# Performance work log

Measured on AMD Instinct MI355X. Metric: run time of the kernel, lower is better.

The kernel has to match this reference:

```python
import jax, jax.numpy as jnp
import numpy as np

D_MODEL = 512; D_STATE = 64; D_CONV = 4; EXPAND = 1; HEADDIM = 128; NGROUPS = 2; CHUNK = 256
D_INNER = EXPAND * (D_MODEL // 2)          # 256
NHEADS = D_INNER // HEADDIM                 # 2
CONV_DIM = D_INNER + 2 * NGROUPS * D_STATE  # 512
D_IN_PROJ = CONV_DIM + NHEADS               # 514

def silu(x):
    return x * jax.nn.sigmoid(x)

def conv1x1(x, w, b):
    # x: (b,c,h,w), w: (o,c)
    return jnp.einsum('bchw,oc->bohw', x, w) + b[None, :, None, None]

def dwconv3x3(x, w, b):
    # depthwise 3x3, SAME padding; w: (c,1,3,3)
    c = x.shape[1]
    y = jax.lax.conv_general_dilated(x, w, (1, 1), 'SAME', feature_group_count=c,
                                     dimension_numbers=('NCHW', 'OIHW', 'NCHW'))
    return y + b[None, :, None, None]

def causal_dwconv1d(x, w, b):
    # x: (b,L,c); w: (c,k). Torch pads k-1 both sides then slices [:L] -> causal left pad.
    k = w.shape[1]
    xp = jnp.pad(x, ((0, 0), (k - 1, 0), (0, 0))).transpose(0, 2, 1)  # (b,c,L+k-1)
    y = jax.lax.conv_general_dilated(xp, w[:, None, :], (1,), 'VALID',
                                     feature_group_count=w.shape[0],
                                     dimension_numbers=('NCH', 'OIH', 'NCH'))
    return y.transpose(0, 2, 1) + b

def axis_attn(x, qw, qb, fw, fb, axis):
    # DualAxisAggAttn single-axis step
    qkv = conv1x1(x, qw, qb)
    c = x.shape[1]
    q, k, v = qkv[:, :1], qkv[:, 1:1 + c], qkv[:, 1 + c:]
    dim = -1 if axis == 'W' else -2
    scores = jax.nn.softmax(q, axis=dim)
    ctx = jnp.sum(k * scores, axis=dim, keepdims=True)
    out = x + jax.nn.sigmoid(v) * ctx
    return conv1x1(out, fw, fb)

def segsum(x):
    # x: (...,T) -> (...,T,T) lower-triangular segment sums, -inf above diagonal
    T = x.shape[-1]
    cs = jnp.cumsum(x, -1)
    d = cs[..., :, None] - cs[..., None, :]
    mask = jnp.tril(jnp.ones((T, T), bool))
    return jnp.where(mask, d, -jnp.inf)

def ssd(X, A, B, C, chunk):
    # Mamba2 SSD chunked scan. X: (b,l,h,p) = x*dt; A: (b,l,h) = dt*A_head; B,C: (b,l,h,n)
    b, l, h, p = X.shape; n = B.shape[-1]; c = l // chunk
    X = X.reshape(b, c, chunk, h, p)
    B = B.reshape(b, c, chunk, h, n)
    C = C.reshape(b, c, chunk, h, n)
    A = A.reshape(b, c, chunk, h).transpose(0, 3, 1, 2)  # (b,h,c,L)
    Acs = jnp.cumsum(A, -1)
    L = jnp.exp(segsum(A))  # (b,h,c,L,L) intra-chunk decay
    Yd = jnp.einsum('bclhn,bcshn,bhcls,bcshp->bclhp', C, B, L, X)
    dec = jnp.exp(Acs[..., -1:] - Acs)
    st = jnp.einsum('bclhn,bhcl,bclhp->bchpn', B, dec, X)  # chunk end-states
    st = jnp.concatenate([jnp.zeros_like(st[:, :1]), st], 1)
    dchunk = jnp.exp(segsum(jnp.pad(Acs[..., -1], ((0, 0), (0, 0), (1, 0)))))
    st = jnp.einsum('bhzc,bchpn->bzhpn', dchunk, st)[:, :-1]  # states entering each chunk
    Yo = jnp.einsum('bclhn,bchpn,bhcl->bclhp', C, st, jnp.exp(Acs))
    return (Yd + Yo).reshape(b, l, h, p)

def setup_inputs() -> dict:
    key = jax.random.key(0)
    ks = jax.random.split(key, 12)
    s = 0.02
    p = {}
    p['u'] = jax.random.normal(ks[0], (8, D_MODEL, 64, 64), jnp.float32)
    p['sc_w1'] = jax.random.normal(ks[1], (D_MODEL, D_MODEL)) * s
    p['sc_b1'] = jnp.zeros((D_MODEL,))
    p['sc_wdw'] = jax.random.normal(ks[2], (D_MODEL, 1, 3, 3)) * s
    p['sc_bdw'] = jnp.zeros((D_MODEL,))
    p['sc_w2'] = jax.random.normal(ks[3], (D_INNER, D_MODEL)) * s
    p['sc_b2'] = jnp.zeros((D_INNER,))
    p['mc_w'] = jax.random.normal(ks[4], (D_INNER, D_MODEL)) * s
    p['mc_b'] = jnp.zeros((D_INNER,))
    p['qkvW_w'] = jax.random.normal(ks[5], (1 + 2 * D_INNER, D_INNER)) * s
    p['qkvW_b'] = jnp.zeros((1 + 2 * D_INNER,))
    p['qkvH_w'] = jax.random.normal(ks[6], (1 + 2 * D_INNER, D_INNER)) * s
    p['qkvH_b'] = jnp.zeros((1 + 2 * D_INNER,))
    p['fuseW_w'] = jax.random.normal(ks[7], (D_INNER, D_INNER)) * s
    p['fuseW_b'] = jnp.zeros((D_INNER,))
    p['fuseH_w'] = jax.random.normal(ks[8], (D_INNER, D_INNER)) * s
    p['fuseH_b'] = jnp.zeros((D_INNER,))
    p['in_proj_w'] = jax.random.normal(ks[9], (D_IN_PROJ, D_INNER)) * s
    p['conv1d_w'] = jax.random.normal(ks[10], (CONV_DIM, D_CONV)) * s
    p['conv1d_b'] = jnp.zeros((CONV_DIM,))
    dt = np.exp(np.linspace(np.log(1e-3), np.log(0.1), NHEADS))
    p['dt_bias'] = jnp.asarray(dt + np.log(-np.expm1(-dt)), jnp.float32)
    p['A_log'] = jnp.asarray(np.log(np.linspace(1.0, 16.0, NHEADS)), jnp.float32)
    p['D'] = jnp.ones((NHEADS,))
    p['norm_w'] = jnp.ones((D_INNER,))
    p['outp_w'] = jax.random.normal(ks[11], (D_MODEL, 2 * D_INNER)) * s
    p['outp_b'] = jnp.zeros((D_MODEL,))
    return p

def reference(u, sc_w1, sc_b1, sc_wdw, sc_bdw, sc_w2, sc_b2, mc_w, mc_b,
              qkvW_w, qkvW_b, qkvH_w, qkvH_b, fuseW_w, fuseW_b, fuseH_w, fuseH_b,
              in_proj_w, conv1d_w, conv1d_b, dt_bias, A_log, D, norm_w, outp_w, outp_b):
    b, _, H, W = u.shape
    # short_conv branch (light_ConvBlock: 1x1 -> dw3x3 -> 1x1, all SiLU; BN folded into bias)
    z = silu(conv1x1(u, sc_w1, sc_b1))
    z = silu(dwconv3x3(z, sc_wdw, sc_bdw))
    z = silu(conv1x1(z, sc_w2, sc_b2))
    # main branch
    x = silu(conv1x1(u, mc_w, mc_b))
    x = axis_attn(x, qkvW_w, qkvW_b, fuseW_w, fuseW_b, 'W')
    x = axis_attn(x, qkvH_w, qkvH_b, fuseH_w, fuseH_b, 'H')
    seqlen = H * W
    u2 = x.transpose(0, 2, 3, 1).reshape(b, seqlen, D_INNER)  # b (h w) c
    xbcdt = u2 @ in_proj_w.T  # (b,l,d_in_proj)
    xBC = xbcdt[..., :CONV_DIM]
    dt = jax.nn.softplus(xbcdt[..., CONV_DIM:] + dt_bias)  # (b,l,h)
    A = -jnp.exp(A_log)  # (h,)
    xBC = silu(causal_dwconv1d(xBC, conv1d_w, conv1d_b))
    xs = xBC[..., :D_INNER]
    Bs = xBC[..., D_INNER:D_INNER + NGROUPS * D_STATE].reshape(b, seqlen, NGROUPS, D_STATE)
    Cs = xBC[..., D_INNER + NGROUPS * D_STATE:].reshape(b, seqlen, NGROUPS, D_STATE)
    Xh = xs.reshape(b, seqlen, NHEADS, HEADDIM)
    rep = NHEADS // NGROUPS
    Bh = jnp.repeat(Bs, rep, axis=2)
    Ch = jnp.repeat(Cs, rep, axis=2)
    y = ssd(Xh * dt[..., None], dt * A[None, None, :], Bh, Ch, CHUNK)
    y = y + Xh * D[None, None, :, None]  # D skip connection
    y = y.reshape(b, seqlen, D_INNER)
    # RMSNormGated with z=None -> plain RMSNorm
    y = y * jax.lax.rsqrt(jnp.mean(y * y, -1, keepdims=True) + 1e-5) * norm_w
    y = y.reshape(b, H, W, D_INNER).transpose(0, 3, 1, 2)
    y = jnp.concatenate([z, y], axis=1)
    return conv1x1(y, outp_w, outp_b)
```

## Files before the change

kernel.cpp:

```cpp
#include <hip/hip_runtime.h>
#include <hip/hip_bf16.h>
#include <cstddef>
#include <cstdint>

#define PTOT 32768
#define HWSZ 4096

typedef __attribute__((ext_vector_type(8))) short bf16x8;
typedef __attribute__((ext_vector_type(4))) short s16x4;
typedef __attribute__((ext_vector_type(4))) float f32x4;

__device__ __forceinline__ float sigf(float x){ return 1.f/(1.f+__expf(-x)); }
__device__ __forceinline__ float siluf(float x){ return x*sigf(x); }
__device__ __forceinline__ short f2b(float x){
  __hip_bfloat16 h = __float2bfloat16(x);
  return *reinterpret_cast<short*>(&h);
}
__device__ __forceinline__ float b2f(short s){
  unsigned u = ((unsigned)(unsigned short)s) << 16;
  return __uint_as_float(u);
}

__device__ __forceinline__ void gload16(const void* g, void* l){
  __builtin_amdgcn_global_load_lds(
      (const __attribute__((address_space(1))) unsigned int*)g,
      (__attribute__((address_space(3))) unsigned int*)l, 16, 0, 0);
}

__global__ __launch_bounds__(256) void k_cvtw(
    const float* __restrict__ s0, const float* __restrict__ s1, const float* __restrict__ s2,
    const float* __restrict__ s3, const float* __restrict__ s4, const float* __restrict__ s5,
    const float* __restrict__ s6, const float* __restrict__ s7, const float* __restrict__ s8,
    short* __restrict__ dst){
  int idx = blockIdx.x*256 + threadIdx.x;
  const float* s; int off;
  if      (idx <  262144){ s=s0; off=idx; }
  else if (idx <  393216){ s=s1; off=idx- 262144; }
  else if (idx <  524288){ s=s2; off=idx- 393216; }
  else if (idx <  655616){ s=s3; off=idx- 524288; }
  else if (idx <  786944){ s=s4; off=idx- 655616; }
  else if (idx <  852480){ s=s5; off=idx- 786944; }
  else if (idx <  918016){ s=s6; off=idx- 852480; }
  else if (idx < 1049600){ s=s7; off=idx- 918016; }
  else if (idx < 1311744){ s=s8; off=idx-1049600; }
  else return;
  dst[idx] = f2b(s[off]);
}

__global__ __launch_bounds__(256) void k_transpose(const float* __restrict__ in, short* __restrict__ out){
  __shared__ float tile[64][33];
  int b = blockIdx.z;
  int c0 = blockIdx.y * 64;
  int s0 = blockIdx.x * 32;
  int tx = threadIdx.x, ty = threadIdx.y;
  const float* ip = in + ((size_t)b*512 + c0)*HWSZ + s0;
  for (int i = ty; i < 64; i += 8) tile[i][tx] = ip[(size_t)i*HWSZ + tx];
  __syncthreads();
  for (int i = ty; i < 32; i += 8){
    unsigned lo = (unsigned)(unsigned short)f2b(tile[2*tx][i]);
    unsigned hi = (unsigned)(unsigned short)f2b(tile[2*tx+1][i]);
    unsigned pk = lo | (hi<<16);
    *reinterpret_cast<unsigned*>(&out[((size_t)((b<<12) + s0 + i))*512 + c0 + 2*tx]) = pk;
  }
}

template<int ACT, int OUT_NCHW>
__global__ __launch_bounds__(256) void k_gemm(
    const short* __restrict__ A0, const short* __restrict__ A1,
    int kSplit, int lda0, int lda1,
    const short* __restrict__ Wt, const float* __restrict__ bias,
    void* __restrict__ Cpv, int N, int K, int ldc, int qkvPerm)
{
  __shared__ short Alds[2][128*32];
  __shared__ short Blds[2][128*32];

  int tid = threadIdx.x;
  int lane = tid & 63;
  int wv = tid >> 6;
  int wr = wv >> 1, wc = wv & 1;
  int lr = lane & 15, lh = lane >> 4;
  int bm = blockIdx.x * 128;
  int bn = blockIdx.y * 128;

  int rl = lane >> 2;
  int kg = (lane & 3) << 3;

  int ar[2], wnr[2];
  #pragma unroll
  for (int j=0;j<2;j++){
    int r = wv*32 + j*16 + rl;
    ar[j] = bm + r;
    int n = bn + r; if (n > N-1) n = N-1;
    wnr[j] = qkvPerm ? ((n==512)?0:(n+1)) : n;
  }

  auto stage = [&](int buf, int k0){
    #pragma unroll
    for (int j=0;j<2;j++){
      const short* asrc;
      if (k0 < kSplit) asrc = A0 + (size_t)ar[j]*lda0 + (k0 + kg);
      else             asrc = A1 + (size_t)ar[j]*lda1 + (k0 - kSplit + kg);
      gload16(asrc, &Alds[buf][(wv*32 + j*16)*32]);
      const short* bsrc = Wt + (size_t)wnr[j]*K + (k0 + kg);
      gload16(bsrc, &Blds[buf][(wv*32 + j*16)*32]);
    }
  };

  f32x4 acc[4][4];
  #pragma unroll
  for (int i=0;i<4;i++)
    #pragma unroll
    for (int j=0;j<4;j++) acc[i][j] = (f32x4){0.f,0.f,0.f,0.f};

  stage(0, 0);
  __syncthreads();
  int NT = K >> 5;
  for (int t=0; t<NT; t++){
    int cur = t & 1;
    if (t+1 < NT) stage(cur^1, (t+1) << 5);
    bf16x8 af[4], bfr[4];
    #pragma unroll
    for (int mi=0;mi<4;mi++)
      af[mi] = *reinterpret_cast<const bf16x8*>(&Alds[cur][(wr*64 + mi*16 + lr)*32 + lh*8]);
    #pragma unroll
    for (int ni=0;ni<4;ni++)
      bfr[ni] = *reinterpret_cast<const bf16x8*>(&Blds[cur][(wc*64 + ni*16 + lr)*32 + lh*8]);
    #pragma unroll
    for (int mi=0;mi<4;mi++)
      #pragma unroll
      for (int ni=0;ni<4;ni++)
        acc[mi][ni] = __builtin_amdgcn_mfma_f32_16x16x32_bf16(af[mi], bfr[ni], acc[mi][ni], 0, 0, 0);
    __syncthreads();
  }

  if (!OUT_NCHW){
    short* Cp = (short*)Cpv;
    #pragma unroll
    for (int mi=0;mi<4;mi++){
      int m = bm + wr*64 + mi*16 + lh*4;
      #pragma unroll
      for (int ni=0;ni<4;ni++){
        int n = bn + wc*64 + ni*16 + lr;
        if (n < N){
          int wn = qkvPerm ? ((n==512)?0:(n+1)) : n;
          float bb = bias ? bias[wn] : 0.f;
          #pragma unroll
          for (int r=0;r<4;r++){
            float v = acc[mi][ni][r] + bb;
            if (ACT==1) v = siluf(v);
            Cp[(size_t)(m+r)*ldc + n] = f2b(v);
          }
        }
      }
    }
  } else {
    float* Cp = (float*)Cpv;
    float* Sep = ((float*)Alds) + wv*16*68;
    #pragma unroll
    for (int mi=0;mi<4;mi++){
      __syncthreads();
      #pragma unroll
      for (int ni=0;ni<4;ni++){
        int n = bn + wc*64 + ni*16 + lr;
        float bb = (bias && n < N) ? bias[n] : 0.f;
        #pragma unroll
        for (int r=0;r<4;r++){
          float v = acc[mi][ni][r] + bb;
          if (ACT==1) v = siluf(v);
          Sep[(lh*4+r)*68 + ni*16 + lr] = v;
        }
      }
      __syncthreads();
      int m = bm + wr*64 + mi*16 + lr;
      size_t mb = ((size_t)(m>>12)*ldc)*HWSZ + (m & 4095);
      #pragma unroll
      for (int g=0; g<16; g++){
        int nl = g*4 + lh;
        float v = Sep[lr*68 + nl];
        int nn = bn + wc*64 + nl;
        if (nn < N) Cp[mb + (size_t)nn*HWSZ] = v;
      }
    }
  }
}

__global__ __launch_bounds__(256) void k_dwconv3x3(const short* __restrict__ in,
    const float* __restrict__ w, const float* __restrict__ bias, short* __restrict__ out){
  int tid = threadIdx.x;
  int cq = tid & 127;
  int wi = tid >> 7;
  int bw = blockIdx.x;
  int b  = bw >> 5;
  int wc = ((bw & 31) << 1) | wi;
  int h0 = blockIdx.y << 4;
  int c  = cq << 2;

  float arr[36];
  {
    const float* wp = &w[c*9];
    #pragma unroll
    for (int t=0;t<9;t++){
      f32x4 v = *reinterpret_cast<const f32x4*>(wp + t*4);
      arr[t*4+0]=v[0]; arr[t*4+1]=v[1]; arr[t*4+2]=v[2]; arr[t*4+3]=v[3];
    }
  }
  f32x4 bias4 = *reinterpret_cast<const f32x4*>(&bias[c]);

  int pb = b << 12;
  auto ldrow = [&](int r, int dw)->f32x4 {
    int ww = wc + dw;
    if ((unsigned)r >= 64u || (unsigned)ww >= 64u) return (f32x4){0.f,0.f,0.f,0.f};
    s16x4 v = *reinterpret_cast<const s16x4*>(&in[((size_t)(pb + (r<<6) + ww) << 9) + c]);
    return (f32x4){b2f(v[0]), b2f(v[1]), b2f(v[2]), b2f(v[3])};
  };

  f32x4 a00,a01,a02,a10,a11,a12,a20,a21,a22;
  a00=ldrow(h0-1,-1); a01=ldrow(h0-1,0); a02=ldrow(h0-1,1);
  a10=ldrow(h0  ,-1); a11=ldrow(h0  ,0); a12=ldrow(h0  ,1);
  #pragma unroll
  for (int hh=0; hh<16; hh++){
    int h = h0 + hh;
    a20=ldrow(h+1,-1); a21=ldrow(h+1,0); a22=ldrow(h+1,1);
    s16x4 o;
    #pragma unroll
    for (int j=0;j<4;j++){
      float v = bias4[j];
      v = fmaf(a00[j], arr[j*9+0], v);
      v = fmaf(a01[j], arr[j*9+1], v);
      v = fmaf(a02[j], arr[j*9+2], v);
      v = fmaf(a10[j], arr[j*9+3], v);
      v = fmaf(a11[j], arr[j*9+4], v);
      v = fmaf(a12[j], arr[j*9+5], v);
      v = fmaf(a20[j], arr[j*9+6], v);
      v = fmaf(a21[j], arr[j*9+7], v);
      v = fmaf(a22[j], arr[j*9+8], v);
      o[j] = f2b(siluf(v));
    }
    *reinterpret_cast<s16x4*>(&out[((size_t)(pb + (h<<6) + wc) << 9) + c]) = o;
    a00=a10; a01=a11; a02=a12;
    a10=a20; a11=a21; a12=a22;
  }
}

__global__ __launch_bounds__(256) void k_attn(const short* __restrict__ x,
    const short* __restrict__ qkv, short* __restrict__ out, int axisH){
  int bl = blockIdx.x;
  int b = bl >> 6, line = bl & 63;
  __shared__ float es[64];
  __shared__ float qs[64];
  int tid = threadIdx.x;
  int pbase = b << 12;
  if (tid < 64){
    int p = axisH ? (pbase | (tid<<6) | line) : (pbase | (line<<6) | tid);
    qs[tid] = b2f(qkv[(size_t)p*520 + 512]);
  }
  __syncthreads();
  float mx = -1e30f;
  for (int t=0;t<64;t++) mx = fmaxf(mx, qs[t]);
  if (tid < 64) es[tid] = __expf(qs[tid]-mx);
  __syncthreads();
  float s = 0.f;
  for (int t=0;t<64;t++) s += es[t];
  float inv = 1.f/s;
  int c = tid;
  float ctx = 0.f;
  for (int t=0;t<64;t++){
    int p = axisH ? (pbase | (t<<6) | line) : (pbase | (line<<6) | t);
    ctx += es[t]*b2f(qkv[(size_t)p*520 + c]);
  }
  ctx *= inv;
  for (int t=0;t<64;t++){
    int p = axisH ? (pbase | (t<<6) | line) : (pbase | (line<<6) | t);
    float vv = b2f(qkv[(size_t)p*520 + 256 + c]);
    float xv = b2f(x[(size_t)p*256 + c]);
    out[(size_t)p*256 + c] = f2b(xv + sigf(vv)*ctx);
  }
}

__global__ __launch_bounds__(256) void k_dt(const short* __restrict__ xbcdt,
    const float* __restrict__ dt_bias, float* __restrict__ dtb){
  int idx = blockIdx.x*256 + threadIdx.x;
  if (idx >= PTOT*2) return;
  int p = idx >> 1, h = idx & 1;
  float xv = b2f(xbcdt[(size_t)p*520 + 512 + h]) + dt_bias[h];
  float sp = (xv > 20.f) ? xv : log1pf(__expf(xv));
  dtb[idx] = sp;
}

__global__ __launch_bounds__(256) void k_conv1d(const short* __restrict__ xbcdt,
    const float* __restrict__ w, const float* __restrict__ bias, short* __restrict__ xBC){
  int tid = threadIdx.x;
  int cq = tid & 127;
  int c  = cq << 2;
  int half = tid >> 7;
  int bs = blockIdx.x;
  int b  = bs >> 7;
  int t0 = ((((bs & 127) << 1) | half) << 4);

  float wk[16];
  {
    const float* wp = &w[c*4];
    #pragma unroll
    for (int t=0;t<4;t++){
      f32x4 v = *reinterpret_cast<const f32x4*>(wp + t*4);
      wk[t*4+0]=v[0]; wk[t*4+1]=v[1]; wk[t*4+2]=v[2]; wk[t*4+3]=v[3];
    }
  }
  f32x4 bias4 = *reinterpret_cast<const f32x4*>(&bias[c]);

  int pb = b << 12;
  auto ld = [&](int t)->f32x4 {
    if (t < 0) return (f32x4){0.f,0.f,0.f,0.f};
    s16x4 v = *reinterpret_cast<const s16x4*>(&xbcdt[(size_t)(pb + t)*520 + c]);
    return (f32x4){b2f(v[0]), b2f(v[1]), b2f(v[2]), b2f(v[3])};
  };

  f32x4 x0,x1,x2,x3;
  x0 = ld(t0-3); x1 = ld(t0-2); x2 = ld(t0-1);
  #pragma unroll
  for (int tt=0; tt<16; tt++){
    int t = t0 + tt;
    x3 = ld(t);
    s16x4 o;
    #pragma unroll
    for (int j=0;j<4;j++){
      float v = bias4[j];
      v = fmaf(x0[j], wk[j*4+0], v);
      v = fmaf(x1[j], wk[j*4+1], v);
      v = fmaf(x2[j], wk[j*4+2], v);
      v = fmaf(x3[j], wk[j*4+3], v);
      o[j] = f2b(siluf(v));
    }
    *reinterpret_cast<s16x4*>(&xBC[((size_t)(pb + t) << 9) + c]) = o;
    x0=x1; x1=x2; x2=x3;
  }
}

__global__ __launch_bounds__(256) void k_ssd_states(
  const short* __restrict__ xBC, const float* __restrict__ dtb, const float* __restrict__ A_log,
  float* __restrict__ states, float* __restrict__ AcsG, float* __restrict__ AtotG)
{
  int ci = blockIdx.x, h = blockIdx.y, b = blockIdx.z;
  int tid = threadIdx.x;
  __shared__ float sa[256], sb[256];
  __shared__ float Bs[64][65];
  __shared__ float Xs[64][136];
  int base = (b<<12) | (ci<<8);
  float Ah = -__expf(A_log[h]);
  sa[tid] = dtb[(size_t)(base + tid)*2 + h] * Ah;
  __syncthreads();
  float* src = sa; float* dst = sb;
  for (int off=1; off<256; off<<=1){
    float v = src[tid];
    if (tid >= off) v += src[tid - off];
    dst[tid] = v;
    __syncthreads();
    float* tswap = src; src = dst; dst = tswap;
  }
  float acs = src[tid];
  float atot = src[255];
  AcsG[((size_t)((b*2+h)*16 + ci))*256 + tid] = acs;
  if (tid == 0) AtotG[(b*2+h)*16 + ci] = atot;

  int tn = tid >> 4;
  int tp = tid & 15;
  float acc[4][8];
  #pragma unroll
  for (int i=0;i<4;i++)
    #pragma unroll
    for (int j=0;j<8;j++) acc[i][j]=0.f;

  for (int t0=0; t0<256; t0+=64){
    __syncthreads();
    for (int e = tid; e < 64*64; e += 256){
      int t = e >> 6, n = e & 63;
      float d = __expf(atot - src[t0 + t]);
      Bs[t][n] = b2f(xBC[(size_t)(base + t0 + t)*512 + 256 + (h<<6) + n]) * d;
    }
    for (int e = tid; e < 64*128; e += 256){
      int t = e >> 7, pp = e & 127;
      Xs[t][pp] = b2f(xBC[(size_t)(base + t0 + t)*512 + (h<<7) + pp]) * dtb[(size_t)(base + t0 + t)*2 + h];
    }
    __syncthreads();
    for (int t=0;t<64;t++){
      float bv[4], xv[8];
      #pragma unroll
      for (int i=0;i<4;i++) bv[i]=Bs[t][tn*4+i];
      #pragma unroll
      for (int j=0;j<8;j++) xv[j]=Xs[t][tp*8+j];
      #pragma unroll
      for (int i=0;i<4;i++)
        #pragma unroll
        for (int j=0;j<8;j++) acc[i][j] = fmaf(bv[i], xv[j], acc[i][j]);
    }
  }
  float* stp = states + (((size_t)(b*16+ci)*2 + h) << 13);
  #pragma unroll
  for (int i=0;i<4;i++){
    float4 s0 = {acc[i][0], acc[i][1], acc[i][2], acc[i][3]};
    float4 s1 = {acc[i][4], acc[i][5], acc[i][6], acc[i][7]};
    float* pdst = &stp[(tn*4+i)*128 + tp*8];
    *reinterpret_cast<float4*>(pdst)   = s0;
    *reinterpret_cast<float4*>(pdst+4) = s1;
  }
}

__global__ __launch_bounds__(256) void k_ssd_scan(const float* __restrict__ states,
    const float* __restrict__ AtotG, float* __restrict__ R){
  int bh = blockIdx.x;
  int b = bh >> 1, h = bh & 1;
  int tid = threadIdx.x;
  float r[32];
  #pragma unroll
  for (int j=0;j<32;j++) r[j]=0.f;
  for (int ci=0; ci<16; ci++){
    size_t off = (((size_t)(b*16+ci)*2) + h) << 13;
    #pragma unroll
    for (int j=0;j<32;j++) R[off + tid + (j<<8)] = r[j];
    if (ci < 15){
      float sc = __expf(AtotG[bh*16 + ci]);
      #pragma unroll
      for (int j=0;j<32;j++) r[j] = fmaf(sc, r[j], states[off + tid + (j<<8)]);
    }
  }
}

__global__ __launch_bounds__(256) void k_ssd_y(
  const short* __restrict__ xBC, const float* __restrict__ dtb,
  const float* __restrict__ AcsG, const float* __restrict__ R,
  const float* __restrict__ Dp, float* __restrict__ yraw)
{
  int bx = blockIdx.x;
  int ci = bx >> 2, lt = bx & 3;
  int h = blockIdx.y, b = blockIdx.z;
  int tid = threadIdx.x, lane = tid & 63, w = tid >> 6;
  int lg = lane >> 4, lr = lane & 15;
  int base = (b<<12) | (ci<<8);
  int l0 = lt << 6;

  __shared__ short Cbf[64*72];
  __shared__ short Bbf[64*72];
  __shared__ short Xt [128*76];
  __shared__ short Sbf[64*72];
  __shared__ float acs_l[64], acs_s[64], dt_s[64];

  const float* acsrow = AcsG + ((size_t)((b*2+h)*16 + ci))*256;

  {
    int row = tid >> 2, c0 = (tid & 3) << 4;
    const short* src = &xBC[(size_t)(base + l0 + row)*512 + 384 + (h<<6) + c0];
    *reinterpret_cast<bf16x8*>(&Cbf[row*72 + c0])     = *reinterpret_cast<const bf16x8*>(src);
    *reinterpret_cast<bf16x8*>(&Cbf[row*72 + c0 + 8]) = *reinterpret_cast<const bf16x8*>(src+8);
  }
  if (tid < 64) acs_l[tid] = acsrow[l0 + tid];

  f32x4 yacc[8];
  #pragma unroll
  for (int pf=0;pf<8;pf++) yacc[pf] = (f32x4){0.f,0.f,0.f,0.f};

  for (int s0 = 0; s0 <= l0; s0 += 64){
    __syncthreads();
    {
      int row = tid >> 2, c0 = (tid & 3) << 4;
      const short* src = &xBC[(size_t)(base + s0 + row)*512 + 256 + (h<<6) + c0];
      *reinterpret_cast<bf16x8*>(&Bbf[row*72 + c0])     = *reinterpret_cast<const bf16x8*>(src);
      *reinterpret_cast<bf16x8*>(&Bbf[row*72 + c0 + 8]) = *reinterpret_cast<const bf16x8*>(src+8);
    }
    {
      int s = tid >> 2;
      int p0 = (tid & 3) << 5;
      const short* src = &xBC[(size_t)(base + s0 + s)*512 + (h<<7) + p0];
      #pragma unroll
      for (int q=0;q<4;q++){
        bf16x8 v = *reinterpret_cast<const bf16x8*>(src + q*8);
        #pragma unroll
        for (int e=0;e<8;e++) Xt[(p0 + q*8 + e)*76 + s] = v[e];
      }
    }
    if (tid < 64){
      acs_s[tid] = acsrow[s0 + tid];
      dt_s[tid]  = dtb[(size_t)(base + s0 + tid)*2 + h];
    }
    __syncthreads();

    f32x4 sacc[4];
    #pragma unroll
    for (int f=0;f<4;f++) sacc[f] = (f32x4){0.f,0.f,0.f,0.f};
    bf16x8 ca0 = *reinterpret_cast<const bf16x8*>(&Cbf[(w*16+lr)*72 + lg*8]);
    bf16x8 ca1 = *reinterpret_cast<const bf16x8*>(&Cbf[(w*16+lr)*72 + 32 + lg*8]);
    #pragma unroll
    for (int f=0;f<4;f++){
      bf16x8 bb0 = *reinterpret_cast<const bf16x8*>(&Bbf[(f*16+lr)*72 + lg*8]);
      bf16x8 bb1 = *reinterpret_cast<const bf16x8*>(&Bbf[(f*16+lr)*72 + 32 + lg*8]);
      sacc[f] = __builtin_amdgcn_mfma_f32_16x16x32_bf16(ca0, bb0, sacc[f], 0, 0, 0);
      sacc[f] = __builtin_amdgcn_mfma_f32_16x16x32_bf16(ca1, bb1, sacc[f], 0, 0, 0);
    }
    #pragma unroll
    for (int f=0;f<4;f++){
      #pragma unroll
      for (int r=0;r<4;r++){
        int ll = w*16 + lg*4 + r;
        int ss = f*16 + lr;
        float v = 0.f;
        if (s0 + ss <= l0 + ll)
          v = sacc[f][r] * __expf(acs_l[ll] - acs_s[ss]) * dt_s[ss];
        Sbf[ll*72 + ss] = f2b(v);
      }
    }
    __syncthreads();

    bf16x8 sa0 = *reinterpret_cast<const bf16x8*>(&Sbf[(w*16+lr)*72 + lg*8]);
    bf16x8 sa1 = *reinterpret_cast<const bf16x8*>(&Sbf[(w*16+lr)*72 + 32 + lg*8]);
    #pragma unroll
    for (int pf=0;pf<8;pf++){
      bf16x8 x0 = *reinterpret_cast<const bf16x8*>(&Xt[(pf*16+lr)*76 + lg*8]);
      bf16x8 x1 = *reinterpret_cast<const bf16x8*>(&Xt[(pf*16+lr)*76 + 32 + lg*8]);
      yacc[pf] = __builtin_amdgcn_mfma_f32_16x16x32_bf16(sa0, x0, yacc[pf], 0, 0, 0);
      yacc[pf] = __builtin_amdgcn_mfma_f32_16x16x32_bf16(sa1, x1, yacc[pf], 0, 0, 0);
    }
  }

  __syncthreads();
  {
    size_t roff = (((size_t)(b*16+ci)*2) + h) << 13;
    int n = tid >> 2;
    const float* src = R + roff + (size_t)n*128;
    #pragma unroll
    for (int j=0;j<8;j++){
      int p = ((tid & 3) << 2) + (j << 4);
      float4 f = *reinterpret_cast<const float4*>(&src[p]);
      Xt[(p+0)*76 + n] = f2b(f.x);
      Xt[(p+1)*76 + n] = f2b(f.y);
      Xt[(p+2)*76 + n] = f2b(f.z);
      Xt[(p+3)*76 + n] = f2b(f.w);
    }
  }
  __syncthreads();
  f32x4 racc[8];
  #pragma unroll
  for (int pf=0;pf<8;pf++) racc[pf] = (f32x4){0.f,0.f,0.f,0.f};
  {
    bf16x8 ca0 = *reinterpret_cast<const bf16x8*>(&Cbf[(w*16+lr)*72 + lg*8]);
    bf16x8 ca1 = *reinterpret_cast<const bf16x8*>(&Cbf[(w*16+lr)*72 + 32 + lg*8]);
    #pragma unroll
    for (int pf=0;pf<8;pf++){
      bf16x8 x0 = *reinterpret_cast<const bf16x8*>(&Xt[(pf*16+lr)*76 + lg*8]);
      bf16x8 x1 = *reinterpret_cast<const bf16x8*>(&Xt[(pf*16+lr)*76 + 32 + lg*8]);
      racc[pf] = __builtin_amdgcn_mfma_f32_16x16x32_bf16(ca0, x0, racc[pf], 0, 0, 0);
      racc[pf] = __builtin_amdgcn_mfma_f32_16x16x32_bf16(ca1, x1, racc[pf], 0, 0, 0);
    }
  }

  float Dh = Dp[h];
  float el[4];
  #pragma unroll
  for (int r=0;r<4;r++) el[r] = __expf(acs_l[w*16 + lg*4 + r]);
  #pragma unroll
  for (int pf=0;pf<8;pf++){
    #pragma unroll
    for (int r=0;r<4;r++){
      int ll = w*16 + lg*4 + r;
      int p = pf*16 + lr;
      size_t pix = (size_t)(base + l0 + ll);
      float xraw = b2f(xBC[pix*512 + (h<<7) + p]);
      yraw[pix*256 + (h<<7) + p] = yacc[pf][r] + el[r]*racc[pf][r] + Dh*xraw;
    }
  }
}

__global__ __launch_bounds__(256) void k_rmsnorm(const float* __restrict__ yraw,
    const float* __restrict__ nw, short* __restrict__ ynorm){
  int p = blockIdx.x;
  int tid = threadIdx.x;
  float v = yraw[(size_t)p*256 + tid];
  float sq = v*v;
  for (int off=32; off; off>>=1) sq += __shfl_down(sq, off);
  __shared__ float wsum[4];
  if ((tid & 63) == 0) wsum[tid>>6] = sq;
  __syncthreads();
  float tot = wsum[0]+wsum[1]+wsum[2]+wsum[3];
  float scale = rsqrtf(tot*(1.f/256.f) + 1e-5f);
  ynorm[(size_t)p*256 + tid] = f2b(v*scale*nw[tid]);
}

extern "C" void kernel_launch(void* const* d_in, const int* in_sizes, int n_in,
                              void* d_out, int out_size, void* d_ws, size_t ws_size,
                              hipStream_t stream)
{
  (void)in_sizes; (void)n_in; (void)out_size; (void)ws_size;
  const float* u        = (const float*)d_in[0];
  const float* sc_w1    = (const float*)d_in[1];
  const float* sc_b1    = (const float*)d_in[2];
  const float* sc_wdw   = (const float*)d_in[3];
  const float* sc_bdw   = (const float*)d_in[4];
  const float* sc_w2    = (const float*)d_in[5];
  const float* sc_b2    = (const float*)d_in[6];
  const float* mc_w     = (const float*)d_in[7];
  const float* mc_b     = (const float*)d_in[8];
  const float* qkvW_w   = (const float*)d_in[9];
  const float* qkvW_b   = (const float*)d_in[10];
  const float* qkvH_w   = (const float*)d_in[11];
  const float* qkvH_b   = (const float*)d_in[12];
  const float* fuseW_w  = (const float*)d_in[13];
  const float* fuseW_b  = (const float*)d_in[14];
  const float* fuseH_w  = (const float*)d_in[15];
  const float* fuseH_b  = (const float*)d_in[16];
  const float* in_proj_w= (const float*)d_in[17];
  const float* conv1d_w = (const float*)d_in[18];
  const float* conv1d_b = (const float*)d_in[19];
  const float* dt_bias  = (const float*)d_in[20];
  const float* A_log    = (const float*)d_in[21];
  const float* Dp       = (const float*)d_in[22];
  const float* norm_w   = (const float*)d_in[23];
  const float* outp_w   = (const float*)d_in[24];
  const float* outp_b   = (const float*)d_in[25];

  char* wsb = (char*)d_ws;
  size_t off = 0;
  auto alloc = [&](size_t bytes){ void* p = wsb + off; off = (off + bytes + 255) & ~(size_t)255; return p; };
  short* wbf   = (short*)alloc((size_t)1311744*2);
  short* slotB = (short*)alloc((size_t)PTOT*520*2);
  short* slotC = (short*)alloc((size_t)PTOT*512*2);
  short* slotZ = (short*)alloc((size_t)PTOT*256*2);
  short* slotE = (short*)alloc((size_t)PTOT*256*2);
  float* slotF = (float*)alloc((size_t)PTOT*256*4);
  float* slotS = (float*)alloc((size_t)4460000*4);

  float* dtb     = slotS;
  float* AcsG    = slotS + 65536;
  float* AtotG   = slotS + 131072;
  float* statesB = slotS + 131328;
  float* Rb      = slotS + 131328 + 2097152;
  short* ynorm   = slotE;
  short* xwh     = (short*)slotF;

  short* w_sc1  = wbf + 0;
  short* w_sc2  = wbf + 262144;
  short* w_mc   = wbf + 393216;
  short* w_qkvW = wbf + 524288;
  short* w_qkvH = wbf + 655616;
  short* w_fuW  = wbf + 786944;
  short* w_fuH  = wbf + 852480;
  short* w_inp  = wbf + 918016;
  short* w_outp = wbf + 1049600;

  short* u_pm = (short*)d_out;
  float* out  = (float*)d_out;

  const int BIG = 1<<30;

  k_cvtw<<<5124, 256, 0, stream>>>(sc_w1, sc_w2, mc_w, qkvW_w, qkvH_w, fuseW_w, fuseH_w, in_proj_w, outp_w, wbf);
  k_transpose<<<dim3(128,8,8), dim3(32,8), 0, stream>>>(u, u_pm);

  k_gemm<1,0><<<dim3(256,4), 256, 0, stream>>>(u_pm, u_pm, BIG, 512, 512, w_sc1, sc_b1, slotB, 512, 512, 512, 0);
  k_dwconv3x3<<<dim3(256,4), 256, 0, stream>>>(slotB, sc_wdw, sc_bdw, slotC);
  k_gemm<1,0><<<dim3(256,2), 256, 0, stream>>>(slotC, slotC, BIG, 512, 512, w_sc2, sc_b2, slotZ, 256, 512, 256, 0);

  k_gemm<1,0><<<dim3(256,2), 256, 0, stream>>>(u_pm, u_pm, BIG, 512, 512, w_mc, mc_b, slotE, 256, 512, 256, 0);
  k_gemm<0,0><<<dim3(256,5), 256, 0, stream>>>(slotE, slotE, BIG, 256, 256, w_qkvW, qkvW_b, slotB, 513, 256, 520, 1);
  k_attn<<<512, 256, 0, stream>>>(slotE, slotB, xwh, 0);
  k_gemm<0,0><<<dim3(256,2), 256, 0, stream>>>(xwh, xwh, BIG, 256, 256, w_fuW, fuseW_b, slotE, 256, 256, 256, 0);
  k_gemm<0,0><<<dim3(256,5), 256, 0, stream>>>(slotE, slotE, BIG, 256, 256, w_qkvH, qkvH_b, slotB, 513, 256, 520, 1);
  k_attn<<<512, 256, 0, stream>>>(slotE, slotB, xwh, 1);
  k_gemm<0,0><<<dim3(256,2), 256, 0, stream>>>(xwh, xwh, BIG, 256, 256, w_fuH, fuseH_b, slotE, 256, 256, 256, 0);

  k_gemm<0,0><<<dim3(256,5), 256, 0, stream>>>(slotE, slotE, BIG, 256, 256, w_inp, nullptr, slotB, 514, 256, 520, 0);
  k_dt<<<256, 256, 0, stream>>>(slotB, dt_bias, dtb);
  k_conv1d<<<1024, 256, 0, stream>>>(slotB, conv1d_w, conv1d_b, slotC);

  k_ssd_states<<<dim3(16,2,8), 256, 0, stream>>>(slotC, dtb, A_log, statesB, AcsG, AtotG);
  k_ssd_scan<<<16, 256, 0, stream>>>(statesB, AtotG, Rb);
  k_ssd_y<<<dim3(64,2,8), 256, 0, stream>>>(slotC, dtb, AcsG, Rb, Dp, slotF);

  k_rmsnorm<<<32768, 256, 0, stream>>>(slotF, norm_w, ynorm);

  k_gemm<0,1><<<dim3(256,4), 256, 0, stream>>>(slotZ, ynorm, 256, 256, 256, w_outp, outp_b, out, 512, 512, 512, 0);
}
```

Measured before the change: 491.9 us.

## Fold fuse 1x1 convs into following projections and triple-buffer GEMM staging

Precomposes the fuseW weights with the qkvH projection and the fuseH weights with in_proj in a new weight-composition kernel. This removes two standalone GEMM launches and their intermediate writes; one wider GEMM now emits both the fused output and the qkvH result. The GEMM main loop also moves from double to triple-buffered LDS with explicit vmcnt waits and one barrier per iteration, to overlap loads with MFMA. The risks are extra bf16 rounding from the composed weights, a larger LDS footprint per block, and a small per-call weight-preprocessing kernel.

```diff
diff --git a/kernel.cpp b/kernel.cpp
--- a/kernel.cpp
+++ b/kernel.cpp
@@ -47,6 +47,48 @@
   dst[idx] = f2b(s[off]);
 }
 
+__global__ __launch_bounds__(256) void k_wcomp(
+    const float* __restrict__ qkvHw, const float* __restrict__ fuWw,
+    const float* __restrict__ fuWb,  const float* __restrict__ qkvHb,
+    const float* __restrict__ inpw,  const float* __restrict__ fuHw,
+    const float* __restrict__ fuHb,
+    short* __restrict__ wcomb, float* __restrict__ bcomb,
+    short* __restrict__ wi2,   float* __restrict__ bi2)
+{
+  int blk = blockIdx.x;
+  int tid = threadIdx.x;
+  __shared__ float as[256];
+  __shared__ float red[256];
+  if (blk < 513){
+    int i = blk;
+    int r = (i==512) ? 0 : (i+1);
+    as[tid]  = qkvHw[(size_t)r*256 + tid];
+    red[tid] = as[tid] * fuWb[tid];
+    __syncthreads();
+    for (int off=128; off; off>>=1){ if (tid<off) red[tid]+=red[tid+off]; __syncthreads(); }
+    float acc = 0.f;
+    #pragma unroll 8
+    for (int k=0;k<256;k++) acc += as[k]*fuWw[(size_t)k*256 + tid];
+    wcomb[(size_t)(256+i)*256 + tid] = f2b(acc);
+    if (tid==0) bcomb[256+i] = red[0] + qkvHb[r];
+  } else if (blk < 769){
+    int j = blk - 513;
+    wcomb[(size_t)j*256 + tid] = f2b(fuWw[(size_t)j*256 + tid]);
+    if (tid==0) bcomb[j] = fuWb[j];
+  } else {
+    int j = blk - 769;
+    as[tid]  = inpw[(size_t)j*256 + tid];
+    red[tid] = as[tid] * fuHb[tid];
+    __syncthreads();
+    for (int off=128; off; off>>=1){ if (tid<off) red[tid]+=red[tid+off]; __syncthreads(); }
+    float acc = 0.f;
+    #pragma unroll 8
+    for (int k=0;k<256;k++) acc += as[k]*fuHw[(size_t)k*256 + tid];
+    wi2[(size_t)j*256 + tid] = f2b(acc);
+    if (tid==0) bi2[j] = red[0];
+  }
+}
+
 __global__ __launch_bounds__(256) void k_transpose(const float* __restrict__ in, short* __restrict__ out){
   __shared__ float tile[64][33];
   int b = blockIdx.z;
@@ -71,8 +113,8 @@
     const short* __restrict__ Wt, const float* __restrict__ bias,
     void* __restrict__ Cpv, int N, int K, int ldc, int qkvPerm)
 {
-  __shared__ short Alds[2][128*32];
-  __shared__ short Blds[2][128*32];
+  __shared__ short Alds[3][128*32];
+  __shared__ short Blds[3][128*32];
 
   int tid = threadIdx.x;
   int lane = tid & 63;
@@ -94,7 +136,8 @@
     wnr[j] = qkvPerm ? ((n==512)?0:(n+1)) : n;
   }
 
-  auto stage = [&](int buf, int k0){
+  auto stage = [&](int buf, int t){
+    int k0 = t << 5;
     #pragma unroll
     for (int j=0;j<2;j++){
       const short* asrc;
@@ -112,12 +155,16 @@
     #pragma unroll
     for (int j=0;j<4;j++) acc[i][j] = (f32x4){0.f,0.f,0.f,0.f};
 
+  int NT = K >> 5;
   stage(0, 0);
-  __syncthreads();
-  int NT = K >> 5;
+  stage(1, 1);
   for (int t=0; t<NT; t++){
-    int cur = t & 1;
-    if (t+1 < NT) stage(cur^1, (t+1) << 5);
+    int cur = t % 3;
+    if (t+1 < NT) asm volatile("s_waitcnt vmcnt(4)" ::: "memory");
+    else          asm volatile("s_waitcnt vmcnt(0)" ::: "memory");
+    __builtin_amdgcn_s_barrier();
+    __builtin_amdgcn_sched_barrier(0);
+    if (t+2 < NT) stage((t+2)%3, t+2);
     bf16x8 af[4], bfr[4];
     #pragma unroll
     for (int mi=0;mi<4;mi++)
@@ -130,7 +177,6 @@
       #pragma unroll
       for (int ni=0;ni<4;ni++)
         acc[mi][ni] = __builtin_amdgcn_mfma_f32_16x16x32_bf16(af[mi], bfr[ni], acc[mi][ni], 0, 0, 0);
-    __syncthreads();
   }
 
   if (!OUT_NCHW){
@@ -242,8 +288,8 @@
   }
 }
 
-__global__ __launch_bounds__(256) void k_attn(const short* __restrict__ x,
-    const short* __restrict__ qkv, short* __restrict__ out, int axisH){
+__global__ __launch_bounds__(256) void k_attn(const short* __restrict__ x, int xld,
+    const short* __restrict__ qkv, int qld, short* __restrict__ out, int axisH){
   int bl = blockIdx.x;
   int b = bl >> 6, line = bl & 63;
   __shared__ float es[64];
@@ -252,7 +298,7 @@
   int pbase = b << 12;
   if (tid < 64){
     int p = axisH ? (pbase | (tid<<6) | line) : (pbase | (line<<6) | tid);
-    qs[tid] = b2f(qkv[(size_t)p*520 + 512]);
+    qs[tid] = b2f(qkv[(size_t)p*qld + 512]);
   }
   __syncthreads();
   float mx = -1e30f;
@@ -266,13 +312,13 @@
   float ctx = 0.f;
   for (int t=0;t<64;t++){
     int p = axisH ? (pbase | (t<<6) | line) : (pbase | (line<<6) | t);
-    ctx += es[t]*b2f(qkv[(size_t)p*520 + c]);
+    ctx += es[t]*b2f(qkv[(size_t)p*qld + c]);
   }
   ctx *= inv;
   for (int t=0;t<64;t++){
     int p = axisH ? (pbase | (t<<6) | line) : (pbase | (line<<6) | t);
-    float vv = b2f(qkv[(size_t)p*520 + 256 + c]);
-    float xv = b2f(x[(size_t)p*256 + c]);
+    float vv = b2f(qkv[(size_t)p*qld + 256 + c]);
+    float xv = b2f(x[(size_t)p*xld + c]);
     out[(size_t)p*256 + c] = f2b(xv + sigf(vv)*ctx);
   }
 }
@@ -618,8 +664,10 @@
   char* wsb = (char*)d_ws;
   size_t off = 0;
   auto alloc = [&](size_t bytes){ void* p = wsb + off; off = (off + bytes + 255) & ~(size_t)255; return p; };
-  short* wbf   = (short*)alloc((size_t)1311744*2);
-  short* slotB = (short*)alloc((size_t)PTOT*520*2);
+  short* wbf   = (short*)alloc((size_t)1640192*2);
+  float* bcomb = (float*)alloc(769*4);
+  float* bi2   = (float*)alloc(514*4);
+  short* slotB = (short*)alloc((size_t)PTOT*776*2);
   short* slotC = (short*)alloc((size_t)PTOT*512*2);
   short* slotZ = (short*)alloc((size_t)PTOT*256*2);
   short* slotE = (short*)alloc((size_t)PTOT*256*2);
@@ -638,11 +686,9 @@
   short* w_sc2  = wbf + 262144;
   short* w_mc   = wbf + 393216;
   short* w_qkvW = wbf + 524288;
-  short* w_qkvH = wbf + 655616;
-  short* w_fuW  = wbf + 786944;
-  short* w_fuH  = wbf + 852480;
-  short* w_inp  = wbf + 918016;
   short* w_outp = wbf + 1049600;
+  short* wcomb  = wbf + 1311744;
+  short* wi2    = wbf + 1311744 + 196864;
 
   short* u_pm = (short*)d_out;
   float* out  = (float*)d_out;
@@ -650,6 +696,8 @@
   const int BIG = 1<<30;
 
   k_cvtw<<<5124, 256, 0, stream>>>(sc_w1, sc_w2, mc_w, qkvW_w, qkvH_w, fuseW_w, fuseH_w, in_proj_w, outp_w, wbf);
+  k_wcomp<<<1283, 256, 0, stream>>>(qkvH_w, fuseW_w, fuseW_b, qkvH_b, in_proj_w, fuseH_w, fuseH_b,
+                                    wcomb, bcomb, wi2, bi2);
   k_transpose<<<dim3(128,8,8), dim3(32,8), 0, stream>>>(u, u_pm);
 
   k_gemm<1,0><<<dim3(256,4), 256, 0, stream>>>(u_pm, u_pm, BIG, 512, 512, w_sc1, sc_b1, slotB, 512, 512, 512, 0);
@@ -658,13 +706,10 @@
 
   k_gemm<1,0><<<dim3(256,2), 256, 0, stream>>>(u_pm, u_pm, BIG, 512, 512, w_mc, mc_b, slotE, 256, 512, 256, 0);
   k_gemm<0,0><<<dim3(256,5), 256, 0, stream>>>(slotE, slotE, BIG, 256, 256, w_qkvW, qkvW_b, slotB, 513, 256, 520, 1);
-  k_attn<<<512, 256, 0, stream>>>(slotE, slotB, xwh, 0);
-  k_gemm<0,0><<<dim3(256,2), 256, 0, stream>>>(xwh, xwh, BIG, 256, 256, w_fuW, fuseW_b, slotE, 256, 256, 256, 0);
-  k_gemm<0,0><<<dim3(256,5), 256, 0, stream>>>(slotE, slotE, BIG, 256, 256, w_qkvH, qkvH_b, slotB, 513, 256, 520, 1);
-  k_attn<<<512, 256, 0, stream>>>(slotE, slotB, xwh, 1);
-  k_gemm<0,0><<<dim3(256,2), 256, 0, stream>>>(xwh, xwh, BIG, 256, 256, w_fuH, fuseH_b, slotE, 256, 256, 256, 0);
-
-  k_gemm<0,0><<<dim3(256,5), 256, 0, stream>>>(slotE, slotE, BIG, 256, 256, w_inp, nullptr, slotB, 514, 256, 520, 0);
+  k_attn<<<512, 256, 0, stream>>>(slotE, 256, slotB, 520, xwh, 0);
+  k_gemm<0,0><<<dim3(256,7), 256, 0, stream>>>(xwh, xwh, BIG, 256, 256, wcomb, bcomb, slotB, 769, 256, 776, 0);
+  k_attn<<<512, 256, 0, stream>>>(slotB, 776, slotB + 256, 776, xwh, 1);
+  k_gemm<0,0><<<dim3(256,5), 256, 0, stream>>>(xwh, xwh, BIG, 256, 256, wi2, bi2, slotB, 514, 256, 520, 0);
   k_dt<<<256, 256, 0, stream>>>(slotB, dt_bias, dtb);
   k_conv1d<<<1024, 256, 0, stream>>>(slotB, conv1d_w, conv1d_b, slotC);
 
```

After: 485.2 us. About the same (-1.4%).
